# Kernel tuning notes

Hardware: AMD Instinct MI355X
Metric: run time of the kernel (lower is better)

The kernel has to match this reference:

```python
import jax, jax.numpy as jnp
import numpy as np

H, F, K, R = 8, 64, 10, 256  # num_heads, in_features, num_sines, num_realizations
B, L = 4, 2048


def setup_inputs() -> dict:
    key = jax.random.key(0)
    k1, k2, k3, k4, k5, k6 = jax.random.split(key, 6)
    return {
        "queries": jax.random.normal(k1, (B, L, H, F), dtype=jnp.float32),
        "keys": jax.random.normal(k2, (B, L, H, F), dtype=jnp.float32),
        "z": jax.random.normal(k3, (B, H, F, 2 * K, R), dtype=jnp.float32),
        "freqs": jax.random.normal(k4, (H, F, K), dtype=jnp.float32),
        "offsets": jax.random.normal(k5, (H, F, K), dtype=jnp.float32),
        "gains": jax.random.normal(k6, (H, F, K), dtype=jnp.float32),
    }


def reference(queries, keys, z, freqs, offsets, gains):
    h, f_dim, k_sines = freqs.shape
    length = queries.shape[1]
    r = z.shape[-1]
    # split positional / non-positional features (rest is empty here: key_dim == in_features)
    q_pos, q_rest = queries[..., :f_dim], queries[..., f_dim:]
    k_pos, k_rest = keys[..., :f_dim], keys[..., f_dim:]

    idx = jnp.arange(length, dtype=queries.dtype)  # linspace(0, L-1, L)
    fr = jax.nn.sigmoid(freqs)[:, :, None, :] / 2.0          # [H, F, 1, K]
    base = 2.0 * jnp.pi * fr * idx[None, None, :, None]       # [H, F, L, K]
    ph_q = base + offsets[:, :, None, :]
    ph_k = base
    # stack(cos, sin) on last axis then flatten -> interleaved cos0,sin0,... : [H, F, L, 2K]
    omega_q = jnp.stack([jnp.cos(ph_q), jnp.sin(ph_q)], axis=-1).reshape(h, f_dim, length, 2 * k_sines)
    omega_k = jnp.stack([jnp.cos(ph_k), jnp.sin(ph_k)], axis=-1).reshape(h, f_dim, length, 2 * k_sines)

    g = jnp.tile(jax.nn.softplus(gains), (1, 1, 2))           # [H, F, 2K] (block-repeated, as in torch .repeat)
    zs = z * g[None, :, :, :, None] / np.sqrt(r * f_dim).astype(np.float32)  # [B, H, F, 2K, R]

    # fused double contraction over f (in_features) and s (2K sines); equals
    # (omega @ z) permuted then multiplied by queries and summed over in_features
    qhat = jnp.einsum('hfls,bhfsr,blhf->blhr', omega_q, zs, q_pos)  # [B, L, H, R]
    khat = jnp.einsum('hfls,bhfsr,blhf->blhr', omega_k, zs, k_pos)

    qhat = jnp.concatenate([qhat, q_rest], axis=-1)
    khat = jnp.concatenate([khat, k_rest], axis=-1)
    return qhat, khat
```

## Files before the change

### kernel.cpp

```cpp
#include <hip/hip_runtime.h>
#include <math.h>


#define NH 8
#define NF 64
#define NK 10
#define NR 256
#define NB 4
#define NL 2048
#define KTOT 1280
#define BK 32
#define NCH (KTOT/BK)
#define NFRAG_B 16
#define WS_BPACK ((size_t)NB*NH*NCH*NFRAG_B*1024)
#define WS_TRIG  ((size_t)NH*NCH*2048*16*4)
#define WS_NEED2 (WS_BPACK + WS_TRIG)

typedef __attribute__((ext_vector_type(8))) short short8;
typedef __attribute__((ext_vector_type(4))) float f32x4;
typedef __attribute__((ext_vector_type(4))) unsigned int u32x4;
typedef __attribute__((ext_vector_type(2))) unsigned int u32x2;

static __device__ __forceinline__ unsigned short f2b(float f) {
    unsigned x = __float_as_uint(f);
    return (unsigned short)((x + 0x7FFFu + ((x >> 16) & 1u)) >> 16);
}
static __device__ __forceinline__ unsigned int pk2(float a, float b) {
    return (unsigned int)f2b(a) | ((unsigned int)f2b(b) << 16);
}
static __device__ __forceinline__ unsigned int cvtpk(float lo, float hi) {
    unsigned int r;
    asm("v_cvt_pk_bf16_f32 %0, %1, %2" : "=v"(r) : "v"(lo), "v"(hi));
    return r;
}
static __device__ __forceinline__ void gload_lds16(const void* g, void* l) {
    __builtin_amdgcn_global_load_lds(
        (const __attribute__((address_space(1))) unsigned int*)g,
        (__attribute__((address_space(3))) unsigned int*)l, 16, 0, 0);
}

__global__ __launch_bounds__(256)
void spe_prep(const float* __restrict__ z, const float* __restrict__ gains,
              unsigned char* __restrict__ bpack)
{
    __shared__ float s_g[NF*NK];
    const int ch  = blockIdx.x;
    const int bh  = blockIdx.y;
    const int h   = bh & 7;
    const int tid = threadIdx.x;
    for (int i = tid; i < NF*NK; i += 256)
        s_g[i] = log1pf(expf(gains[h*NF*NK + i])) * 0.0078125f;
    __syncthreads();
    const float* zb = z + (size_t)bh * KTOT * NR;
    unsigned char* dst = bpack + ((size_t)(bh*NCH + ch) * NFRAG_B) * 1024;
    #pragma unroll
    for (int it = 0; it < 4; ++it) {
        const int s  = tid + 256*it;
        const int fi = s >> 6;
        const int l  = s & 63;
        const int r  = fi*16 + (l & 15);
        const int k0 = ch*BK + (l >> 4)*8;
        u32x4 wv;
        #pragma unroll
        for (int jp = 0; jp < 4; ++jp) {
            const int ka = k0 + 2*jp, kb = ka + 1;
            const int fa = (ka*3277) >> 16; int sa = ka - fa*20; if (sa >= NK) sa -= NK;
            const int fb = (kb*3277) >> 16; int sb = kb - fb*20; if (sb >= NK) sb -= NK;
            const float va = zb[(size_t)ka*NR + r] * s_g[fa*NK + sa];
            const float vb = zb[(size_t)kb*NR + r] * s_g[fb*NK + sb];
            wv[jp] = pk2(va, vb);
        }
        *(u32x4*)(dst + (size_t)s*16) = wv;
    }
}

__global__ __launch_bounds__(256)
void spe_trig(const float* __restrict__ freqs, unsigned int* __restrict__ trig)
{
    const int t = blockIdx.x;
    const int h = blockIdx.y;
    const int tid = threadIdx.x;
    #pragma unroll
    for (int it = 0; it < 32; ++it) {
        const int site = tid + 256*it;
        const int l  = site >> 2;
        const int jg = site & 3;
        u32x4 wv;
        #pragma unroll
        for (int j = 0; j < 4; ++j) {
            const int kidx2 = t*16 + jg*4 + j;
            const float fv = freqs[h*640 + kidx2];
            const float fr = 0.5f / (1.0f + expf(-fv));
            const float x  = __builtin_amdgcn_fractf(fr * (float)l);
            wv[j] = pk2(__builtin_amdgcn_cosf(x), __builtin_amdgcn_sinf(x));
        }
        *(u32x4*)(trig + ((size_t)(h*NCH + t)*2048 + l)*16 + jg*4) = wv;
    }
}

#define OFF2_B   0
#define OFF2_A   49152
#define OFF2_POS 81920
#define OFF2_CS  114688
#define SMEM2_SZ 119808

__global__ __launch_bounds__(1024, 4)
void spe_main2(const float* __restrict__ queries, const float* __restrict__ keys,
               const float* __restrict__ offsets,
               const unsigned char* __restrict__ bpack,
               const unsigned int* __restrict__ trig,
               float* __restrict__ out)
{
    __shared__ __attribute__((aligned(16))) unsigned char smem[SMEM2_SZ];
    const int tid  = threadIdx.x;
    const int lane = tid & 63;
    const int w    = tid >> 6;

    const int bid = blockIdx.x;
    const int swz = (bid & 7) * 64 + (bid >> 3);
    const int l0  = (swz & 15) * 128;
    const int bh  = swz >> 4;
    const int b = bh >> 3, h = bh & 7;

    float2* ld_cs = (float2*)(smem + OFF2_CS);
    unsigned short* pos_t = (unsigned short*)(smem + OFF2_POS);

    for (int i = tid; i < NF*NK; i += 1024) {
        const float xo = __builtin_amdgcn_fractf(offsets[h*640 + i] * 0.15915494309189535f);
        ld_cs[i] = make_float2(__builtin_amdgcn_cosf(xo), __builtin_amdgcn_sinf(xo));
    }
    {
        const int row = tid & 127;
        const int qk  = (tid >> 7) & 1;
        const int fg  = tid >> 8;
        const float* src = (qk ? keys : queries)
            + ((size_t)((b*NL + l0 + row)*NH + h))*NF + fg*16;
        unsigned short* pd = pos_t + qk*8192 + (fg*16)*128 + row;
        #pragma unroll
        for (int jj = 0; jj < 4; ++jj) {
            const float4 v = *(const float4*)(src + jj*4);
            pd[(jj*4+0)*128] = f2b(v.x);
            pd[(jj*4+1)*128] = f2b(v.y);
            pd[(jj*4+2)*128] = f2b(v.z);
            pd[(jj*4+3)*128] = f2b(v.w);
        }
    }
    __syncthreads();

    const unsigned char* bp = bpack + (size_t)bh * ((size_t)NCH*NFRAG_B*1024);
    const unsigned int*  tp = trig  + (size_t)h  * ((size_t)NCH*2048*16);

    const int wq = w >> 2, wn = w & 3;
    const int sqk  = w >> 3;
    const int soct = (w >> 1) & 3;
    const int srq  = ((w & 1) << 6) | lane;
    const unsigned short* posm = pos_t + sqk*8192;
    const int a_w = ((sqk*8 + (srq >> 4)) << 10) + ((soct*16 + (srq & 15)) << 4);
    const size_t t_off = ((size_t)(l0 + srq))*16 + soct*4;

    f32x4 acc[4][4];
    #pragma unroll
    for (int mi = 0; mi < 4; ++mi)
        #pragma unroll
        for (int ni = 0; ni < 4; ++ni)
            acc[mi][ni] = (f32x4){0.f, 0.f, 0.f, 0.f};

    u32x4 trA = *(const u32x4*)(tp + t_off);
    gload_lds16(bp + (size_t)w*1024 + (size_t)lane*16, smem + OFF2_B + (w << 10));
    u32x4 trB;

    auto synthA = [&](int tt, const u32x4& tr, int apar) {
        u32x4 av;
        #pragma unroll
        for (int p = 0; p < 4; ++p) {
            const int kidx2 = tt*16 + soct*4 + p;
            const int f = (kidx2 * 6554) >> 16;
            const float ck = __uint_as_float(tr[p] << 16);
            const float sk = __uint_as_float(tr[p] & 0xffff0000u);
            const float pv = __uint_as_float(((unsigned)posm[f*128 + srq]) << 16);
            float c, s;
            if (sqk == 0) {
                const float2 cs = ld_cs[kidx2];
                c = ck*cs.x - sk*cs.y;
                s = sk*cs.x + ck*cs.y;
            } else { c = ck; s = sk; }
            av[p] = cvtpk(c*pv, s*pv);
        }
        *(u32x4*)(smem + OFF2_A + apar*16384 + a_w) = av;
    };

    auto mfmaStep = [&](int bsel_, int apar) {
        const unsigned char* Bc = smem + OFF2_B + bsel_*16384;
        short8 bf[4];
        #pragma unroll
        for (int ni = 0; ni < 4; ++ni)
            bf[ni] = *(const short8*)(Bc + ((wn*4 + ni) << 10) + (lane << 4));
        const unsigned char* Ac = smem + OFF2_A + apar*16384;
        #pragma unroll
        for (int mi = 0; mi < 4; ++mi) {
            const short8 af = *(const short8*)(Ac + ((wq*4 + mi) << 10) + (lane << 4));
            #pragma unroll
            for (int ni = 0; ni < 4; ++ni)
                acc[mi][ni] = __builtin_amdgcn_mfma_f32_16x16x32_bf16(af, bf[ni], acc[mi][ni], 0, 0, 0);
        }
    };

    int bsel = 0;
    #pragma unroll 1
    for (int t = 0; t < NCH; t += 2) {
        {
            const int tn = t + 1;
            const int wb = (bsel + 1 == 3) ? 0 : bsel + 1;
            trB = *(const u32x4*)(tp + (size_t)tn*2048*16 + t_off);
            gload_lds16(bp + ((size_t)tn*NFRAG_B + w)*1024 + (size_t)lane*16,
                        smem + OFF2_B + wb*16384 + (w << 10));
            asm volatile("s_waitcnt vmcnt(2)" ::: "memory");
            __builtin_amdgcn_sched_barrier(0);
            synthA(t, trA, 0);
            asm volatile("s_waitcnt lgkmcnt(0)" ::: "memory");
            __builtin_amdgcn_sched_barrier(0);
            __builtin_amdgcn_s_barrier();
            mfmaStep(bsel, 0);
            bsel = wb;
        }
        {
            const int tn = (t + 2 < NCH) ? t + 2 : NCH - 1;
            const int wb = (bsel + 1 == 3) ? 0 : bsel + 1;
            trA = *(const u32x4*)(tp + (size_t)tn*2048*16 + t_off);
            gload_lds16(bp + ((size_t)tn*NFRAG_B + w)*1024 + (size_t)lane*16,
                        smem + OFF2_B + wb*16384 + (w << 10));
            asm volatile("s_waitcnt vmcnt(2)" ::: "memory");
            __builtin_amdgcn_sched_barrier(0);
            synthA(t + 1, trB, 1);
            asm volatile("s_waitcnt lgkmcnt(0)" ::: "memory");
            __builtin_amdgcn_sched_barrier(0);
            __builtin_amdgcn_s_barrier();
            mfmaStep(bsel, 1);
            bsel = wb;
        }
    }

    const size_t qk_off = (size_t)(wq >> 1) * ((size_t)NB*NL*NH*NR);
    const int mbase = l0 + (wq & 1) * 64;
    const int row_l = (lane >> 4) * 4;
    const int col_r = lane & 15;
    #pragma unroll
    for (int mi = 0; mi < 4; ++mi) {
        const int lg = mbase + mi*16 + row_l;
        #pragma unroll
        for (int ni = 0; ni < 4; ++ni) {
            const int rg = wn*64 + ni*16 + col_r;
            const f32x4 v = acc[mi][ni];
            #pragma unroll
            for (int q = 0; q < 4; ++q)
                out[qk_off + ((size_t)((b*NL + lg + q)*NH + h))*NR + rg] = v[q];
        }
    }
}

#define OFF_B   0
#define OFF_A   49152
#define OFF_POS 57344
#define OFF_FR  73728
#define OFF_CO  76288
#define OFF_SO  78848
#define SMEM_SZ 81408

__global__ __launch_bounds__(512, 4)
void spe_main(const float* __restrict__ queries, const float* __restrict__ keys,
              const float* __restrict__ freqs, const float* __restrict__ offsets,
              const unsigned char* __restrict__ bpack, float* __restrict__ out)
{
    __shared__ __attribute__((aligned(16))) unsigned char smem[SMEM_SZ];
    const int tid  = threadIdx.x;
    const int lane = tid & 63;
    const int w    = tid >> 6;
    const int l0   = blockIdx.x * 64;
    const int bh   = blockIdx.y;
    const int b = bh >> 3, h = bh & 7;

    float* ld_fr = (float*)(smem + OFF_FR);
    float* ld_co = (float*)(smem + OFF_CO);
    float* ld_so = (float*)(smem + OFF_SO);
    unsigned short* pos_t = (unsigned short*)(smem + OFF_POS);

    for (int i = tid; i < NF*NK; i += 512) {
        const float fv = freqs[h*NF*NK + i];
        ld_fr[i] = 0.5f / (1.0f + expf(-fv));
        const float xo = __builtin_amdgcn_fractf(offsets[h*NF*NK + i] * 0.15915494309189535f);
        ld_co[i] = __builtin_amdgcn_cosf(xo);
        ld_so[i] = __builtin_amdgcn_sinf(xo);
    }
    {
        const int r  = tid >> 2;
        const int f0 = (tid & 3) * 16;
        const int rl = r & 63;
        const float* src = (r < 64)
            ? queries + ((size_t)((b*NL + l0 + rl)*NH + h))*NF + f0
            : keys    + ((size_t)((b*NL + l0 + rl)*NH + h))*NF + f0;
        unsigned short* pdst = pos_t + ((r >> 6) << 12);
        #pragma unroll
        for (int j = 0; j < 4; ++j) {
            const float4 v = *(const float4*)(src + j*4);
            const int f = f0 + j*4;
            pdst[(f+0)*64 + rl] = f2b(v.x);
            pdst[(f+1)*64 + rl] = f2b(v.y);
            pdst[(f+2)*64 + rl] = f2b(v.z);
            pdst[(f+3)*64 + rl] = f2b(v.w);
        }
    }
    __syncthreads();

    const unsigned char* bp = bpack + (size_t)bh * ((size_t)NCH*NFRAG_B*1024);
    const int fi0 = w*2;
    gload_lds16(bp + (size_t)fi0*1024 + lane*16,               smem + OFF_B + (fi0  <<10));
    gload_lds16(bp + (size_t)(fi0+1)*1024 + lane*16,           smem + OFF_B + ((fi0+1)<<10));
    gload_lds16(bp + (size_t)(NFRAG_B + fi0)*1024 + lane*16,   smem + OFF_B + 16384 + (fi0  <<10));
    gload_lds16(bp + (size_t)(NFRAG_B + fi0+1)*1024 + lane*16, smem + OFF_B + 16384 + ((fi0+1)<<10));

    const int wm = w >> 2, wn = w & 3;
    f32x4 acc[4][4];
    #pragma unroll
    for (int mi = 0; mi < 4; ++mi)
        #pragma unroll
        for (int ni = 0; ni < 4; ++ni)
            acc[mi][ni] = (f32x4){0.f, 0.f, 0.f, 0.f};

    const int rq   = ((w & 1) << 5) | (lane & 31);
    const int oct  = w >> 1;
    const int half = lane >> 5;
    const float lf = (float)(l0 + rq);
    const unsigned short* posq = pos_t;
    const unsigned short* posk = pos_t + 4096;
    const int aw_q = OFF_A + ((rq >> 4) << 10) + ((oct*16 + (rq & 15)) << 4) + (half << 3);
    const int aw_k = aw_q + 4096;

    auto synthA = [&](int t, u32x2& q01, u32x2& k01) {
        #pragma unroll
        for (int p = 0; p < 2; ++p) {
            const int kk   = t*BK + oct*8 + half*4 + p*2;
            const int f    = (kk*3277) >> 16;
            const int srem = kk - f*20;
            const int kidx = f*NK + (srem >> 1);
            const float x  = __builtin_amdgcn_fractf(ld_fr[kidx] * lf);
            const float ck = __builtin_amdgcn_cosf(x);
            const float sk = __builtin_amdgcn_sinf(x);
            const float co = ld_co[kidx], so = ld_so[kidx];
            const float cq = ck*co - sk*so;
            const float sq = sk*co + ck*so;
            const float pq = __uint_as_float(((unsigned)posq[f*64 + rq]) << 16);
            const float pk = __uint_as_float(((unsigned)posk[f*64 + rq]) << 16);
            q01[p] = cvtpk(cq*pq, sq*pq);
            k01[p] = cvtpk(ck*pk, sk*pk);
        }
    };

    u32x2 q01, k01;
    synthA(0, q01, k01);

    int bsel  = 0;
    int bsel2 = 2;
    for (int t = 0; t < NCH; ++t) {
        if (t < NCH-1) { asm volatile("s_waitcnt vmcnt(2)" ::: "memory"); }
        else           { asm volatile("s_waitcnt vmcnt(0)" ::: "memory"); }
        __builtin_amdgcn_sched_barrier(0);
        __builtin_amdgcn_s_barrier();

        if (t + 2 < NCH) {
            unsigned char* Bn = smem + OFF_B + bsel2*16384;
            gload_lds16(bp + (size_t)((t+2)*NFRAG_B + fi0)*1024 + lane*16,
                        Bn + (fi0<<10));
            gload_lds16(bp + (size_t)((t+2)*NFRAG_B + fi0+1)*1024 + lane*16,
                        Bn + ((fi0+1)<<10));
        }

        *(u32x2*)(smem + aw_q) = q01;
        *(u32x2*)(smem + aw_k) = k01;
        asm volatile("s_waitcnt lgkmcnt(0)" ::: "memory");
        __builtin_amdgcn_sched_barrier(0);
        __builtin_amdgcn_s_barrier();

        const unsigned char* Bc = smem + OFF_B + bsel*16384;
        short8 bf[4];
        #pragma unroll
        for (int ni = 0; ni < 4; ++ni)
            bf[ni] = *(const short8*)(Bc + ((wn*4 + ni) << 10) + (lane << 4));

        if (t + 1 < NCH) synthA(t + 1, q01, k01);

        #pragma unroll
        for (int mi = 0; mi < 4; ++mi) {
            const short8 af = *(const short8*)(smem + OFF_A + ((wm*4 + mi) << 10) + (lane << 4));
            #pragma unroll
            for (int ni = 0; ni < 4; ++ni)
                acc[mi][ni] = __builtin_amdgcn_mfma_f32_16x16x32_bf16(af, bf[ni], acc[mi][ni], 0, 0, 0);
        }

        bsel  = (bsel  == 2) ? 0 : bsel  + 1;
        bsel2 = (bsel2 == 2) ? 0 : bsel2 + 1;
    }

    const size_t qk_off = (size_t)wm * ((size_t)NB*NL*NH*NR);
    const int row_l = (lane >> 4) * 4;
    const int col_r = lane & 15;
    #pragma unroll
    for (int mi = 0; mi < 4; ++mi) {
        const int lg = l0 + mi*16 + row_l;
        #pragma unroll
        for (int ni = 0; ni < 4; ++ni) {
            const int rg = wn*64 + ni*16 + col_r;
            const f32x4 v = acc[mi][ni];
            #pragma unroll
            for (int q = 0; q < 4; ++q)
                out[qk_off + ((size_t)((b*NL + lg + q)*NH + h))*NR + rg] = v[q];
        }
    }
}

extern "C" void kernel_launch(void* const* d_in, const int* in_sizes, int n_in,
                              void* d_out, int out_size, void* d_ws, size_t ws_size,
                              hipStream_t stream) {
    const float* queries = (const float*)d_in[0];
    const float* keys    = (const float*)d_in[1];
    const float* z       = (const float*)d_in[2];
    const float* freqs   = (const float*)d_in[3];
    const float* offsets = (const float*)d_in[4];
    const float* gains   = (const float*)d_in[5];
    float* out = (float*)d_out;

    unsigned char* bpack = (unsigned char*)d_ws;
    spe_prep<<<dim3(NCH, NB*NH), 256, 0, stream>>>(z, gains, bpack);

    if (ws_size >= WS_NEED2) {
        unsigned int* trig = (unsigned int*)(bpack + WS_BPACK);
        spe_trig<<<dim3(NCH, NH), 256, 0, stream>>>(freqs, trig);
        spe_main2<<<dim3(512), 1024, 0, stream>>>(queries, keys, offsets, bpack, trig, out);
    } else {
        spe_main<<<dim3(NL/64, NB*NH), 512, 0, stream>>>(queries, keys, freqs, offsets, bpack, out);
    }
}
```

Baseline: 145.7 us.

## Halve block tile to 64 rows, double-buffer B, and synthesize A in registers ahead

Replaces the 1024-thread, 128-row main kernel with a 512-thread, 64-row variant that launches twice as many blocks and uses less LDS per block. B tiles go from triple to double buffering, with each wave loading two fragments. The A operand for the next chunk is synthesized in registers while the current MFMAs run, with one barrier per chunk instead of split phases. The aim is more resident blocks and better overlap of trig synthesis with MFMA. The cost is that B-panel reuse per block drops, so global B traffic doubles, and the block index mapping changes L2 locality.

```diff
diff --git a/kernel.cpp b/kernel.cpp
--- a/kernel.cpp
+++ b/kernel.cpp
@@ -98,65 +98,71 @@
     }
 }
 
-#define OFF2_B   0
-#define OFF2_A   49152
-#define OFF2_POS 81920
-#define OFF2_CS  114688
-#define SMEM2_SZ 119808
-
-__global__ __launch_bounds__(1024, 4)
-void spe_main2(const float* __restrict__ queries, const float* __restrict__ keys,
+#define OFF3_B   0
+#define OFF3_A   32768
+#define OFF3_POS 49152
+#define OFF3_CS  65536
+#define SMEM3_SZ 70656
+
+__global__ __launch_bounds__(512, 4)
+void spe_main3(const float* __restrict__ queries, const float* __restrict__ keys,
                const float* __restrict__ offsets,
                const unsigned char* __restrict__ bpack,
                const unsigned int* __restrict__ trig,
                float* __restrict__ out)
 {
-    __shared__ __attribute__((aligned(16))) unsigned char smem[SMEM2_SZ];
+    __shared__ __attribute__((aligned(16))) unsigned char smem[SMEM3_SZ];
     const int tid  = threadIdx.x;
     const int lane = tid & 63;
     const int w    = tid >> 6;
 
-    const int bid = blockIdx.x;
-    const int swz = (bid & 7) * 64 + (bid >> 3);
-    const int l0  = (swz & 15) * 128;
-    const int bh  = swz >> 4;
-    const int b = bh >> 3, h = bh & 7;
-
-    float2* ld_cs = (float2*)(smem + OFF2_CS);
-    unsigned short* pos_t = (unsigned short*)(smem + OFF2_POS);
-
-    for (int i = tid; i < NF*NK; i += 1024) {
+    const int fb = blockIdx.x;
+    const int h  = fb & 7;
+    const int b  = (fb >> 3) & 3;
+    const int l0 = (fb >> 5) * 64;
+    const int bh = b*NH + h;
+
+    float2* ld_cs = (float2*)(smem + OFF3_CS);
+    unsigned short* pos_t = (unsigned short*)(smem + OFF3_POS);
+
+    for (int i = tid; i < NF*NK; i += 512) {
         const float xo = __builtin_amdgcn_fractf(offsets[h*640 + i] * 0.15915494309189535f);
         ld_cs[i] = make_float2(__builtin_amdgcn_cosf(xo), __builtin_amdgcn_sinf(xo));
     }
     {
-        const int row = tid & 127;
-        const int qk  = (tid >> 7) & 1;
-        const int fg  = tid >> 8;
-        const float* src = (qk ? keys : queries)
-            + ((size_t)((b*NL + l0 + row)*NH + h))*NF + fg*16;
-        unsigned short* pd = pos_t + qk*8192 + (fg*16)*128 + row;
-        #pragma unroll
-        for (int jj = 0; jj < 4; ++jj) {
-            const float4 v = *(const float4*)(src + jj*4);
-            pd[(jj*4+0)*128] = f2b(v.x);
-            pd[(jj*4+1)*128] = f2b(v.y);
-            pd[(jj*4+2)*128] = f2b(v.z);
-            pd[(jj*4+3)*128] = f2b(v.w);
-        }
-    }
-    __syncthreads();
+        const int r  = tid >> 2;
+        const int f0 = (tid & 3) * 16;
+        const int rl = r & 63;
+        const float* src = (r < 64)
+            ? queries + ((size_t)((b*NL + l0 + rl)*NH + h))*NF + f0
+            : keys    + ((size_t)((b*NL + l0 + rl)*NH + h))*NF + f0;
+        unsigned short* pdst = pos_t + ((r >> 6) << 12);
+        #pragma unroll
+        for (int j = 0; j < 4; ++j) {
+            const float4 v = *(const float4*)(src + j*4);
+            const int f = f0 + j*4;
+            pdst[(f+0)*64 + rl] = f2b(v.x);
+            pdst[(f+1)*64 + rl] = f2b(v.y);
+            pdst[(f+2)*64 + rl] = f2b(v.z);
+            pdst[(f+3)*64 + rl] = f2b(v.w);
+        }
+    }
 
     const unsigned char* bp = bpack + (size_t)bh * ((size_t)NCH*NFRAG_B*1024);
     const unsigned int*  tp = trig  + (size_t)h  * ((size_t)NCH*2048*16);
 
-    const int wq = w >> 2, wn = w & 3;
-    const int sqk  = w >> 3;
-    const int soct = (w >> 1) & 3;
-    const int srq  = ((w & 1) << 6) | lane;
-    const unsigned short* posm = pos_t + sqk*8192;
-    const int a_w = ((sqk*8 + (srq >> 4)) << 10) + ((soct*16 + (srq & 15)) << 4);
-    const size_t t_off = ((size_t)(l0 + srq))*16 + soct*4;
+    const int wq   = w >> 2;
+    const int wn   = w & 3;
+    const size_t tstep = (size_t)2048*16;
+    const unsigned int* tbase = tp + (size_t)(l0 + lane)*16 + wn*4;
+    const int a_w  = ((wq*4 + (lane >> 4)) << 10) + ((wn*16 + (lane & 15)) << 4);
+    const int fi0  = w * 2;
+
+    u32x4 trCur = *(const u32x4*)(tbase);
+    gload_lds16(bp + (size_t)fi0*1024 + lane*16,     smem + OFF3_B + (fi0  << 10));
+    gload_lds16(bp + (size_t)(fi0+1)*1024 + lane*16, smem + OFF3_B + ((fi0+1) << 10));
+    u32x4 trNxt = *(const u32x4*)(tbase + tstep);
+    __syncthreads();
 
     f32x4 acc[4][4];
     #pragma unroll
@@ -165,88 +171,77 @@
         for (int ni = 0; ni < 4; ++ni)
             acc[mi][ni] = (f32x4){0.f, 0.f, 0.f, 0.f};
 
-    u32x4 trA = *(const u32x4*)(tp + t_off);
-    gload_lds16(bp + (size_t)w*1024 + (size_t)lane*16, smem + OFF2_B + (w << 10));
-    u32x4 trB;
-
-    auto synthA = [&](int tt, const u32x4& tr, int apar) {
+    auto synthA = [&](int t, const u32x4 tr) -> u32x4 {
         u32x4 av;
+        const int kb = t*16 + wn*4;
         #pragma unroll
         for (int p = 0; p < 4; ++p) {
-            const int kidx2 = tt*16 + soct*4 + p;
-            const int f = (kidx2 * 6554) >> 16;
+            const int kidx = kb + p;
+            const int f    = (kidx * 6554) >> 16;
             const float ck = __uint_as_float(tr[p] << 16);
             const float sk = __uint_as_float(tr[p] & 0xffff0000u);
-            const float pv = __uint_as_float(((unsigned)posm[f*128 + srq]) << 16);
+            const float pv = __uint_as_float(((unsigned)pos_t[wq*4096 + f*64 + lane]) << 16);
             float c, s;
-            if (sqk == 0) {
-                const float2 cs = ld_cs[kidx2];
+            if (wq == 0) {
+                const float2 cs = ld_cs[kidx];
                 c = ck*cs.x - sk*cs.y;
                 s = sk*cs.x + ck*cs.y;
             } else { c = ck; s = sk; }
             av[p] = cvtpk(c*pv, s*pv);
         }
-        *(u32x4*)(smem + OFF2_A + apar*16384 + a_w) = av;
+        return av;
     };
 
-    auto mfmaStep = [&](int bsel_, int apar) {
-        const unsigned char* Bc = smem + OFF2_B + bsel_*16384;
+    u32x4 av = synthA(0, trCur);
+
+    #pragma unroll 2
+    for (int t = 0; t < NCH; ++t) {
+        const int par = t & 1;
+
+        *(u32x4*)(smem + OFF3_A + par*8192 + a_w) = av;
+        asm volatile("s_waitcnt lgkmcnt(0)" ::: "memory");
+        if (t == NCH-1) { asm volatile("s_waitcnt vmcnt(0)" ::: "memory"); }
+        else            { asm volatile("s_waitcnt vmcnt(1)" ::: "memory"); }
+        __builtin_amdgcn_sched_barrier(0);
+        __builtin_amdgcn_s_barrier();
+        __builtin_amdgcn_sched_barrier(0);
+
+        if (t + 1 < NCH) {
+            unsigned char* Bn = smem + OFF3_B + ((t+1) & 1)*16384;
+            gload_lds16(bp + ((size_t)(t+1)*NFRAG_B + fi0)*1024 + lane*16,
+                        Bn + (fi0 << 10));
+            gload_lds16(bp + ((size_t)(t+1)*NFRAG_B + fi0+1)*1024 + lane*16,
+                        Bn + ((fi0+1) << 10));
+        }
+        u32x4 trTmp;
+        if (t + 2 < NCH) trTmp = *(const u32x4*)(tbase + (size_t)(t+2)*tstep);
+        __builtin_amdgcn_sched_barrier(0);
+
+        const unsigned char* Bc = smem + OFF3_B + par*16384;
         short8 bf[4];
         #pragma unroll
         for (int ni = 0; ni < 4; ++ni)
             bf[ni] = *(const short8*)(Bc + ((wn*4 + ni) << 10) + (lane << 4));
-        const unsigned char* Ac = smem + OFF2_A + apar*16384;
+
+        if (t + 1 < NCH) av = synthA(t + 1, trNxt);
+
         #pragma unroll
         for (int mi = 0; mi < 4; ++mi) {
-            const short8 af = *(const short8*)(Ac + ((wq*4 + mi) << 10) + (lane << 4));
+            const short8 af = *(const short8*)(smem + OFF3_A + par*8192
+                                               + ((wq*4 + mi) << 10) + (lane << 4));
             #pragma unroll
             for (int ni = 0; ni < 4; ++ni)
                 acc[mi][ni] = __builtin_amdgcn_mfma_f32_16x16x32_bf16(af, bf[ni], acc[mi][ni], 0, 0, 0);
         }
-    };
-
-    int bsel = 0;
-    #pragma unroll 1
-    for (int t = 0; t < NCH; t += 2) {
-        {
-            const int tn = t + 1;
-            const int wb = (bsel + 1 == 3) ? 0 : bsel + 1;
-            trB = *(const u32x4*)(tp + (size_t)tn*2048*16 + t_off);
-            gload_lds16(bp + ((size_t)tn*NFRAG_B + w)*1024 + (size_t)lane*16,
-                        smem + OFF2_B + wb*16384 + (w << 10));
-            asm volatile("s_waitcnt vmcnt(2)" ::: "memory");
-            __builtin_amdgcn_sched_barrier(0);
-            synthA(t, trA, 0);
-            asm volatile("s_waitcnt lgkmcnt(0)" ::: "memory");
-            __builtin_amdgcn_sched_barrier(0);
-            __builtin_amdgcn_s_barrier();
-            mfmaStep(bsel, 0);
-            bsel = wb;
-        }
-        {
-            const int tn = (t + 2 < NCH) ? t + 2 : NCH - 1;
-            const int wb = (bsel + 1 == 3) ? 0 : bsel + 1;
-            trA = *(const u32x4*)(tp + (size_t)tn*2048*16 + t_off);
-            gload_lds16(bp + ((size_t)tn*NFRAG_B + w)*1024 + (size_t)lane*16,
-                        smem + OFF2_B + wb*16384 + (w << 10));
-            asm volatile("s_waitcnt vmcnt(2)" ::: "memory");
-            __builtin_amdgcn_sched_barrier(0);
-            synthA(t + 1, trB, 1);
-            asm volatile("s_waitcnt lgkmcnt(0)" ::: "memory");
-            __builtin_amdgcn_sched_barrier(0);
-            __builtin_amdgcn_s_barrier();
-            mfmaStep(bsel, 1);
-            bsel = wb;
-        }
-    }
-
-    const size_t qk_off = (size_t)(wq >> 1) * ((size_t)NB*NL*NH*NR);
-    const int mbase = l0 + (wq & 1) * 64;
+        if (t + 2 < NCH) trNxt = trTmp;
+    }
+
+    const size_t qk_off = (size_t)wq * ((size_t)NB*NL*NH*NR);
     const int row_l = (lane >> 4) * 4;
     const int col_r = lane & 15;
     #pragma unroll
     for (int mi = 0; mi < 4; ++mi) {
-        const int lg = mbase + mi*16 + row_l;
+        const int lg = l0 + mi*16 + row_l;
         #pragma unroll
         for (int ni = 0; ni < 4; ++ni) {
             const int rg = wn*64 + ni*16 + col_r;
@@ -434,7 +429,7 @@
     if (ws_size >= WS_NEED2) {
         unsigned int* trig = (unsigned int*)(bpack + WS_BPACK);
         spe_trig<<<dim3(NCH, NH), 256, 0, stream>>>(freqs, trig);
-        spe_main2<<<dim3(512), 1024, 0, stream>>>(queries, keys, offsets, bpack, trig, out);
+        spe_main3<<<dim3(1024), 512, 0, stream>>>(queries, keys, offsets, bpack, trig, out);
     } else {
         spe_main<<<dim3(NL/64, NB*NH), 512, 0, stream>>>(queries, keys, freqs, offsets, bpack, out);
     }
```

After: 141.2 us. -3.1%, faster.
